# Kernel tuning notes

Hardware: AMD Instinct MI355X
Metric: run time of the kernel (lower is better)

## Reference

```python
import jax, jax.numpy as jnp
import numpy as np

NF = 10      # num RBF / Chebyshev features
GAMMA = 1.0
EMB = 10
H = 64
NHEADS = 2


def _rbf(d):
    centers = jnp.arange(1, NF + 1, dtype=d.dtype)
    return jnp.exp(-GAMMA * (centers - d[..., None]) ** 2)


def _cheb(a):
    feats = [jnp.ones_like(a), a]
    for _ in range(2, NF):
        feats.append(2 * a * feats[-1] - feats[-2])
    return jnp.stack(feats, -1)


def _gru_layer(xs, wih, whh, bih, bhh):
    # xs: [L, B, D] -> [L, B, H]; PyTorch gate order r, z, n
    B = xs.shape[1]
    def step(h, xt):
        gi = xt @ wih.T + bih
        gh = h @ whh.T + bhh
        ir, iz, inn = jnp.split(gi, 3, -1)
        hr, hz, hn = jnp.split(gh, 3, -1)
        r = jax.nn.sigmoid(ir + hr)
        z = jax.nn.sigmoid(iz + hz)
        n = jnp.tanh(inn + r * hn)
        hnew = (1 - z) * n + z * h
        return hnew, hnew
    h0 = jnp.zeros((B, H), xs.dtype)
    _, ys = jax.lax.scan(step, h0, xs)
    return ys


def _mha(x, in_w, in_b, out_w, out_b):
    B, L, E = x.shape
    hd = E // NHEADS
    qkv = x @ in_w.T + in_b
    q, k, v = jnp.split(qkv, 3, -1)
    sp = lambda t: t.reshape(B, L, NHEADS, hd).transpose(0, 2, 1, 3)
    q, k, v = sp(q), sp(k), sp(v)
    scale = 1.0 / float(np.sqrt(hd))
    att = jax.nn.softmax(jnp.einsum('bhqd,bhkd->bhqk', q, k) * scale, -1)
    o = jnp.einsum('bhqk,bhkd->bhqd', att, v).transpose(0, 2, 1, 3).reshape(B, L, E)
    return o @ out_w.T + out_b


def _ln(x, s, b):
    m = x.mean(-1, keepdims=True)
    v = ((x - m) ** 2).mean(-1, keepdims=True)
    return (x - m) / jnp.sqrt(v + 1e-5) * s + b


def setup_inputs() -> dict:
    key = jax.random.key(0)
    ks = jax.random.split(key, 48)
    N, L = 384, 256
    # bond rows: [atom_idx1, atom_idx2, bond_dist]; angle rows: [d1, d2, angle]
    idx1 = jax.random.randint(ks[0], (N, L), 1, 119).astype(jnp.float32)
    idx2 = jax.random.randint(ks[1], (N, L), 1, 119).astype(jnp.float32)
    dist = jax.random.uniform(ks[2], (N, L), minval=0.5, maxval=5.0)
    d1 = jax.random.uniform(ks[3], (N, L), minval=0.5, maxval=5.0)
    d2 = jax.random.uniform(ks[4], (N, L), minval=0.5, maxval=5.0)
    ang = jax.random.uniform(ks[5], (N, L), minval=-1.0, maxval=1.0)
    bond_x = jnp.stack([idx1, idx2, dist], 1)
    angle_x = jnp.stack([d1, d2, ang], 1)
    is_angle = (jnp.arange(N) % 3 == 2)
    x = jnp.where(is_angle[:, None, None], angle_x, bond_x)

    def nrm(k, shp, s=0.1):
        return jax.random.normal(k, shp) * s

    D_IN = 2 * EMB + NF  # 30
    inp = {
        'x': x,
        'emb': nrm(ks[6], (119, EMB), 1.0),
        'wih0': nrm(ks[7], (3 * H, D_IN)),
        'whh0': nrm(ks[8], (3 * H, H)),
        'bih0': nrm(ks[9], (3 * H,)),
        'bhh0': nrm(ks[10], (3 * H,)),
        'wih12': nrm(ks[11], (2, 3 * H, H)),
        'whh12': nrm(ks[12], (2, 3 * H, H)),
        'bih12': nrm(ks[13], (2, 3 * H)),
        'bhh12': nrm(ks[14], (2, 3 * H)),
        'in_w1': nrm(ks[15], (3 * H, H)),
        'in_b1': nrm(ks[16], (3 * H,)),
        'out_w1': nrm(ks[17], (H, H)),
        'out_b1': nrm(ks[18], (H,)),
        'in_w2': nrm(ks[19], (3 * H, H)),
        'in_b2': nrm(ks[20], (3 * H,)),
        'out_w2': nrm(ks[21], (H, H)),
        'out_b2': nrm(ks[22], (H,)),
        'ff_w1': nrm(ks[23], (1024, H)),
        'ff_b1': nrm(ks[24], (1024,)),
        'ff_w2': nrm(ks[25], (H, 1024)),
        'ff_b2': nrm(ks[26], (H,)),
        'ln1_s': jnp.ones((H,)), 'ln1_b': jnp.zeros((H,)),
        'ln2_s': jnp.ones((H,)), 'ln2_b': jnp.zeros((H,)),
        'ln3_s': jnp.ones((H,)), 'ln3_b': jnp.zeros((H,)),
        'ln4_s': jnp.ones((H,)), 'ln4_b': jnp.zeros((H,)),
        'fw1': nrm(ks[27], (256, H)), 'fb1': nrm(ks[28], (256,)),
        'fw2': nrm(ks[29], (64, 256)), 'fb2': nrm(ks[30], (64,)),
        'fw3': nrm(ks[31], (32, 64)), 'fb3': nrm(ks[32], (32,)),
        'fw4': nrm(ks[33], (1, 32)), 'fb4': nrm(ks[34], (1,)),
    }
    return inp


def reference(x, emb, wih0, whh0, bih0, bhh0, wih12, whh12, bih12, bhh12,
              in_w1, in_b1, out_w1, out_b1, in_w2, in_b2, out_w2, out_b2,
              ff_w1, ff_b1, ff_w2, ff_b2,
              ln1_s, ln1_b, ln2_s, ln2_b, ln3_s, ln3_b, ln4_s, ln4_b,
              fw1, fb1, fw2, fb2, fw3, fb3, fw4, fb4):
    # Vectorized featurization (replaces the per-triplet Python loop):
    # rows with i%3 in {0,1} are bond rows, i%3==2 are angle rows.
    i1 = jnp.clip(x[:, 0].astype(jnp.int32), 0, 118)
    i2 = jnp.clip(x[:, 1].astype(jnp.int32), 0, 118)
    bond_feat = jnp.concatenate([emb[i1], emb[i2], _rbf(x[:, 2])], -1)
    angle_feat = jnp.concatenate([_rbf(x[:, 0]), _rbf(x[:, 1]), _cheb(x[:, 2])], -1)
    is_angle = (jnp.arange(x.shape[0]) % 3 == 2)
    feat = jnp.where(is_angle[:, None, None], angle_feat, bond_feat)  # [N, L, 30]

    hs = feat.transpose(1, 0, 2)  # [L, N, 30]
    hs = _gru_layer(hs, wih0, whh0, bih0, bhh0)
    for l in range(2):
        hs = _gru_layer(hs, wih12[l], whh12[l], bih12[l], bhh12[l])
    g = hs.transpose(1, 0, 2)  # [N, L, H]

    def ffn(t):
        return jax.nn.relu(jax.nn.relu(t @ ff_w1.T + ff_b1) @ ff_w2.T + ff_b2)

    a = _mha(g, in_w1, in_b1, out_w1, out_b1)
    h = _ln(g + a, ln1_s, ln1_b)
    h = _ln(h + ffn(h), ln2_s, ln2_b)
    a = _mha(h, in_w2, in_b2, out_w2, out_b2)
    h = _ln(a + a, ln3_s, ln3_b)  # faithful to original: attn_out + attn_out
    h = _ln(h + ffn(h), ln4_s, ln4_b)
    o = h[:, -1, :]
    o = jax.nn.silu(o @ fw1.T + fb1)
    o = jax.nn.silu(o @ fw2.T + fb2)
    o = jax.nn.silu(o @ fw3.T + fb3)
    o = o @ fw4.T + fb4
    return o.squeeze(-1)
```

## Files before the change

### kernel.cpp

```cpp
#include <hip/hip_runtime.h>

static constexpr int NB   = 384;
static constexpr int SEQL = 256;
static constexpr int NROWS = NB * SEQL;

typedef short bf16x8 __attribute__((ext_vector_type(8)));
typedef float f32x4  __attribute__((ext_vector_type(4)));

union B8u {
    bf16x8 v;
    ushort us[8];
    uint4  q;
};

union F4u { float4 v; float f[4]; };

__device__ inline ushort f2bf(float f) {
    uint u = __float_as_uint(f);
    uint r = u + 0x7FFFu + ((u >> 16) & 1u);
    return (ushort)(r >> 16);
}

__device__ inline void split8(float4 a, float4 b, B8u& hi, B8u& lo) {
    float f[8] = {a.x, a.y, a.z, a.w, b.x, b.y, b.z, b.w};
    #pragma unroll
    for (int i = 0; i < 8; ++i) {
        ushort h = f2bf(f[i]);
        hi.us[i] = h;
        float fh = __uint_as_float(((uint)h) << 16);
        lo.us[i] = f2bf(f[i] - fh);
    }
}

__device__ inline float fast_rcp(float x) {
    float r = __builtin_amdgcn_rcpf(x);
    return r * (2.f - x * r);
}
__device__ inline float fast_sig(float x) {
    float e = __expf(fminf(-x, 80.f));
    return fast_rcp(1.f + e);
}
__device__ inline float fast_tanh(float a) {
    float e = __expf(fminf(2.f * fabsf(a), 80.f));
    float t = 1.f - 2.f * fast_rcp(1.f + e);
    return (a >= 0.f) ? t : -t;
}

__device__ inline void split1(const float* s, ushort* h, ushort* l, int i) {
    float f = s[i];
    ushort hh = f2bf(f);
    h[i] = hh;
    l[i] = f2bf(f - __uint_as_float(((uint)hh) << 16));
}

__global__ __launch_bounds__(256) void split_all(
    const float* s0, const float* s1, const float* s2, const float* s3,
    const float* s4, const float* s5, const float* s6, const float* s7,
    const float* s8,
    ushort* h0, ushort* h1, ushort* h2, ushort* h3, ushort* h4,
    ushort* h5, ushort* h6, ushort* h7, ushort* h8,
    ushort* l0, ushort* l1, ushort* l2, ushort* l3, ushort* l4,
    ushort* l5, ushort* l6, ushort* l7, ushort* l8)
{
    const int b = blockIdx.x;
    const float* s; ushort* h; ushort* l; int base;
    if      (b < 256) { s = s0; h = h0; l = l0; base = 0; }
    else if (b < 512) { s = s1; h = h1; l = l1; base = 256; }
    else if (b < 608) { s = s2; h = h2; l = l2; base = 512; }
    else if (b < 656) { s = s3; h = h3; l = l3; base = 608; }
    else if (b < 704) { s = s4; h = h4; l = l4; base = 656; }
    else if (b < 720) { s = s5; h = h5; l = l5; base = 704; }
    else if (b < 736) { s = s6; h = h6; l = l6; base = 720; }
    else if (b < 784) { s = s7; h = h7; l = l7; base = 736; }
    else              { s = s8; h = h8; l = l8; base = 784; }
    split1(s, h, l, (b - base) * 256 + threadIdx.x);
}

__global__ __launch_bounds__(192) void featproj_kernel(
    const float* __restrict__ x, const float* __restrict__ emb,
    const float* __restrict__ wih0, const float* __restrict__ bih0,
    float* __restrict__ X)
{
    __shared__ float F[32][33];
    const int tid = threadIdx.x;
    const int m0  = blockIdx.x * 32;

    if (tid < 96) {
        const int r   = tid & 31;
        const int grp = tid >> 5;
        const int m   = m0 + r;
        const int b   = m % NB;
        const int l   = m / NB;
        const float* xb = x + (size_t)b * (3 * SEQL);
        const float x0 = xb[l], x1 = xb[SEQL + l], x2 = xb[2 * SEQL + l];
        const bool is_angle = (b % 3) == 2;
        float o[10];
        if (is_angle) {
            if (grp < 2) {
                const float a = (grp == 0) ? x0 : x1;
                #pragma unroll
                for (int c = 0; c < 10; ++c) { float d = (float)(c + 1) - a; o[c] = __expf(-d * d); }
            } else {
                float t0 = 1.f, t1 = x2;
                o[0] = 1.f; o[1] = x2;
                #pragma unroll
                for (int c = 2; c < 10; ++c) { float t = 2.f * x2 * t1 - t0; o[c] = t; t0 = t1; t1 = t; }
            }
        } else {
            if (grp < 2) {
                const float xv = (grp == 0) ? x0 : x1;
                int idx = (int)xv; idx = idx < 0 ? 0 : (idx > 118 ? 118 : idx);
                #pragma unroll
                for (int c = 0; c < 10; ++c) o[c] = emb[idx * 10 + c];
            } else {
                #pragma unroll
                for (int c = 0; c < 10; ++c) { float d = (float)(c + 1) - x2; o[c] = __expf(-d * d); }
            }
        }
        #pragma unroll
        for (int c = 0; c < 10; ++c) F[r][grp * 10 + c] = o[c];
    }
    __syncthreads();

    float w[30];
    #pragma unroll
    for (int k = 0; k < 30; ++k) w[k] = wih0[tid * 30 + k];
    const float bj = bih0[tid];
    for (int r = 0; r < 32; ++r) {
        float acc = bj;
        #pragma unroll
        for (int k = 0; k < 30; ++k) acc += F[r][k] * w[k];
        X[(size_t)(m0 + r) * 192 + tid] = acc;
    }
}

__global__ __launch_bounds__(256, 1) void gru_mfma(
    const float* __restrict__ X, const ushort* __restrict__ WhhHi,
    const ushort* __restrict__ WhhLo, const float* __restrict__ bhh,
    float* __restrict__ Y, int out_batch_major)
{
    constexpr int PAD = 88;
    __shared__ __align__(16) ushort Hh[2][16][PAD];
    __shared__ __align__(16) ushort Hl[2][16][PAD];

    const int tid  = threadIdx.x;
    const int wt   = tid >> 6;
    const int lane = tid & 63;
    const int c    = lane & 15;
    const int g    = lane >> 4;
    const int b0   = blockIdx.x * 16;

    B8u awh[3][2], awl[3][2];
    #pragma unroll
    for (int gam = 0; gam < 3; ++gam)
        #pragma unroll
        for (int ks = 0; ks < 2; ++ks) {
            size_t off = (size_t)(64 * gam + 16 * wt + c) * 64 + 32 * ks + 8 * g;
            awh[gam][ks].q = *(const uint4*)(WhhHi + off);
            awl[gam][ks].q = *(const uint4*)(WhhLo + off);
        }
    float bg[3][4];
    #pragma unroll
    for (int gam = 0; gam < 3; ++gam)
        #pragma unroll
        for (int r = 0; r < 4; ++r)
            bg[gam][r] = bhh[64 * gam + 16 * wt + 4 * g + r];

    {
        ushort* zh = &Hh[0][0][0];
        ushort* zl = &Hl[0][0][0];
        for (int i = tid; i < 2 * 16 * PAD; i += 256) { zh[i] = 0; zl[i] = 0; }
    }
    float hold[4] = {0.f, 0.f, 0.f, 0.f};

    F4u gi[3];
    {
        const float* xp = X + ((size_t)(b0 + c)) * 192;
        #pragma unroll
        for (int gam = 0; gam < 3; ++gam)
            gi[gam].v = *(const float4*)(xp + 64 * gam + 16 * wt + 4 * g);
    }
    __syncthreads();

    for (int t = 0; t < SEQL; ++t) {
        const int p = t & 1;

        B8u bh[2], bl[2];
        #pragma unroll
        for (int ks = 0; ks < 2; ++ks) {
            const int sl = (4 * ks + g) ^ (c & 7);
            bh[ks].q = *(const uint4*)&Hh[p][c][sl * 8];
            bl[ks].q = *(const uint4*)&Hl[p][c][sl * 8];
        }

        f32x4 a0[3], a1[3];
        #pragma unroll
        for (int gam = 0; gam < 3; ++gam) {
            a0[gam] = (f32x4){bg[gam][0], bg[gam][1], bg[gam][2], bg[gam][3]};
            a1[gam] = (f32x4){0.f, 0.f, 0.f, 0.f};
        }
        #pragma unroll
        for (int gam = 0; gam < 3; ++gam) {
            a0[gam] = __builtin_amdgcn_mfma_f32_16x16x32_bf16(awh[gam][0].v, bh[0].v, a0[gam], 0, 0, 0);
            a1[gam] = __builtin_amdgcn_mfma_f32_16x16x32_bf16(awh[gam][1].v, bh[1].v, a1[gam], 0, 0, 0);
            a0[gam] = __builtin_amdgcn_mfma_f32_16x16x32_bf16(awl[gam][0].v, bh[0].v, a0[gam], 0, 0, 0);
            a1[gam] = __builtin_amdgcn_mfma_f32_16x16x32_bf16(awl[gam][1].v, bh[1].v, a1[gam], 0, 0, 0);
            a0[gam] = __builtin_amdgcn_mfma_f32_16x16x32_bf16(awh[gam][0].v, bl[0].v, a0[gam], 0, 0, 0);
            a1[gam] = __builtin_amdgcn_mfma_f32_16x16x32_bf16(awh[gam][1].v, bl[1].v, a1[gam], 0, 0, 0);
        }

        F4u ngi[3];
        {
            const int tn = (t + 1 < SEQL) ? t + 1 : t;
            const float* xp = X + ((size_t)tn * NB + b0 + c) * 192;
            #pragma unroll
            for (int gam = 0; gam < 3; ++gam)
                ngi[gam].v = *(const float4*)(xp + 64 * gam + 16 * wt + 4 * g);
        }

        float hn4[4];
        #pragma unroll
        for (int r = 0; r < 4; ++r) {
            const float gr = a0[0][r] + a1[0][r];
            const float gz = a0[1][r] + a1[1][r];
            const float gn = a0[2][r] + a1[2][r];
            const float rr = fast_sig(gi[0].f[r] + gr);
            const float zz = fast_sig(gi[1].f[r] + gz);
            const float nn = fast_tanh(gi[2].f[r] + rr * gn);
            hn4[r] = (1.f - zz) * nn + zz * hold[r];
            hold[r] = hn4[r];
        }

        {
            const size_t row = out_batch_major ? ((size_t)(b0 + c) * SEQL + t)
                                               : ((size_t)t * NB + b0 + c);
            *(float4*)&Y[row * 64 + 16 * wt + 4 * g] =
                make_float4(hn4[0], hn4[1], hn4[2], hn4[3]);
        }

        {
            ushort hh[4], hl[4];
            #pragma unroll
            for (int r = 0; r < 4; ++r) {
                ushort h = f2bf(hn4[r]);
                hh[r] = h;
                hl[r] = f2bf(hn4[r] - __uint_as_float(((uint)h) << 16));
            }
            const int sl = (2 * wt + (g >> 1)) ^ (c & 7);
            const int ad = sl * 8 + (g & 1) * 4;
            *(uint2*)&Hh[p ^ 1][c][ad] = make_uint2((uint)hh[0] | ((uint)hh[1] << 16),
                                                    (uint)hh[2] | ((uint)hh[3] << 16));
            *(uint2*)&Hl[p ^ 1][c][ad] = make_uint2((uint)hl[0] | ((uint)hl[1] << 16),
                                                    (uint)hl[2] | ((uint)hl[3] << 16));
        }
        #pragma unroll
        for (int gam = 0; gam < 3; ++gam) gi[gam].v = ngi[gam].v;

        asm volatile("s_waitcnt lgkmcnt(0)" ::: "memory");
        __builtin_amdgcn_sched_barrier(0);
        __builtin_amdgcn_s_barrier();
        __builtin_amdgcn_sched_barrier(0);
    }
}

template<int NCOLS>
__global__ __launch_bounds__(256, 2) void gemm_mfma(
    const float* __restrict__ A, const ushort* __restrict__ Whi,
    const ushort* __restrict__ Wlo, const float* __restrict__ bias,
    float* __restrict__ C)
{
    const int tid = threadIdx.x;
    const int w   = tid >> 6;
    const int lane = tid & 63;
    const int c = lane & 15;
    const int g = lane >> 4;
    const int m0 = blockIdx.x * 128 + 32 * w;

    B8u ah[2][2], al[2][2];
    #pragma unroll
    for (int rm = 0; rm < 2; ++rm) {
        const float* ap = A + (size_t)(m0 + 16 * rm + c) * 64;
        #pragma unroll
        for (int ks = 0; ks < 2; ++ks) {
            float4 v0 = *(const float4*)(ap + 32 * ks + 8 * g);
            float4 v1 = *(const float4*)(ap + 32 * ks + 8 * g + 4);
            split8(v0, v1, ah[rm][ks], al[rm][ks]);
        }
    }

    f32x4 acc[NCOLS / 16][2];
    #pragma unroll
    for (int nt = 0; nt < NCOLS / 16; ++nt) {
        float bv = bias[16 * nt + c];
        #pragma unroll
        for (int rm = 0; rm < 2; ++rm)
            acc[nt][rm] = (f32x4){bv, bv, bv, bv};
    }

    #pragma unroll
    for (int nt = 0; nt < NCOLS / 16; ++nt) {
        B8u wh[2], wl[2];
        #pragma unroll
        for (int ks = 0; ks < 2; ++ks) {
            size_t off = (size_t)(16 * nt + c) * 64 + 32 * ks + 8 * g;
            wh[ks].q = *(const uint4*)(Whi + off);
            wl[ks].q = *(const uint4*)(Wlo + off);
        }
        #pragma unroll
        for (int rm = 0; rm < 2; ++rm)
            #pragma unroll
            for (int ks = 0; ks < 2; ++ks) {
                acc[nt][rm] = __builtin_amdgcn_mfma_f32_16x16x32_bf16(ah[rm][ks].v, wh[ks].v, acc[nt][rm], 0, 0, 0);
                acc[nt][rm] = __builtin_amdgcn_mfma_f32_16x16x32_bf16(al[rm][ks].v, wh[ks].v, acc[nt][rm], 0, 0, 0);
                acc[nt][rm] = __builtin_amdgcn_mfma_f32_16x16x32_bf16(ah[rm][ks].v, wl[ks].v, acc[nt][rm], 0, 0, 0);
            }
    }

    #pragma unroll
    for (int nt = 0; nt < NCOLS / 16; ++nt)
        #pragma unroll
        for (int rm = 0; rm < 2; ++rm)
            #pragma unroll
            for (int reg = 0; reg < 4; ++reg) {
                int row = m0 + 16 * rm + 4 * g + reg;
                C[(size_t)row * NCOLS + 16 * nt + c] = acc[nt][rm][reg];
            }
}

__global__ __launch_bounds__(256, 2) void gemm_ln_mfma(
    const float* __restrict__ A, const ushort* __restrict__ Whi,
    const ushort* __restrict__ Wlo, const float* __restrict__ bias,
    const float* __restrict__ resid,
    const float* __restrict__ lns, const float* __restrict__ lnb,
    float* __restrict__ O)
{
    const int tid = threadIdx.x;
    const int w   = tid >> 6;
    const int lane = tid & 63;
    const int c = lane & 15;
    const int g = lane >> 4;
    const int m0 = blockIdx.x * 128 + 32 * w;

    B8u ah[2][2], al[2][2];
    #pragma unroll
    for (int rm = 0; rm < 2; ++rm) {
        const float* ap = A + (size_t)(m0 + 16 * rm + c) * 64;
        #pragma unroll
        for (int ks = 0; ks < 2; ++ks) {
            float4 v0 = *(const float4*)(ap + 32 * ks + 8 * g);
            float4 v1 = *(const float4*)(ap + 32 * ks + 8 * g + 4);
            split8(v0, v1, ah[rm][ks], al[rm][ks]);
        }
    }

    f32x4 acc[4][2];
    #pragma unroll
    for (int nt = 0; nt < 4; ++nt) {
        float bv = bias[16 * nt + c];
        #pragma unroll
        for (int rm = 0; rm < 2; ++rm)
            acc[nt][rm] = (f32x4){bv, bv, bv, bv};
    }

    #pragma unroll
    for (int nt = 0; nt < 4; ++nt) {
        B8u wh[2], wl[2];
        #pragma unroll
        for (int ks = 0; ks < 2; ++ks) {
            size_t off = (size_t)(16 * nt + c) * 64 + 32 * ks + 8 * g;
            wh[ks].q = *(const uint4*)(Whi + off);
            wl[ks].q = *(const uint4*)(Wlo + off);
        }
        #pragma unroll
        for (int rm = 0; rm < 2; ++rm)
            #pragma unroll
            for (int ks = 0; ks < 2; ++ks) {
                acc[nt][rm] = __builtin_amdgcn_mfma_f32_16x16x32_bf16(ah[rm][ks].v, wh[ks].v, acc[nt][rm], 0, 0, 0);
                acc[nt][rm] = __builtin_amdgcn_mfma_f32_16x16x32_bf16(al[rm][ks].v, wh[ks].v, acc[nt][rm], 0, 0, 0);
                acc[nt][rm] = __builtin_amdgcn_mfma_f32_16x16x32_bf16(ah[rm][ks].v, wl[ks].v, acc[nt][rm], 0, 0, 0);
            }
    }

    float vv[4][2][4];
    #pragma unroll
    for (int nt = 0; nt < 4; ++nt)
        #pragma unroll
        for (int rm = 0; rm < 2; ++rm)
            #pragma unroll
            for (int reg = 0; reg < 4; ++reg) {
                const int row = m0 + 16 * rm + 4 * g + reg;
                const float a = acc[nt][rm][reg];
                const float r_ = resid ? resid[(size_t)row * 64 + 16 * nt + c] : a;
                vv[nt][rm][reg] = a + r_;
            }

    float sv[4], bv[4];
    #pragma unroll
    for (int nt = 0; nt < 4; ++nt) { sv[nt] = lns[16 * nt + c]; bv[nt] = lnb[16 * nt + c]; }

    #pragma unroll
    for (int rm = 0; rm < 2; ++rm)
        #pragma unroll
        for (int reg = 0; reg < 4; ++reg) {
            float sum = vv[0][rm][reg] + vv[1][rm][reg] + vv[2][rm][reg] + vv[3][rm][reg];
            float sq  = vv[0][rm][reg]*vv[0][rm][reg] + vv[1][rm][reg]*vv[1][rm][reg]
                      + vv[2][rm][reg]*vv[2][rm][reg] + vv[3][rm][reg]*vv[3][rm][reg];
            #pragma unroll
            for (int off = 1; off < 16; off <<= 1) {
                sum += __shfl_xor(sum, off);
                sq  += __shfl_xor(sq,  off);
            }
            const float mean = sum * (1.f / 64.f);
            const float var  = sq * (1.f / 64.f) - mean * mean;
            const float inv  = rsqrtf(var + 1e-5f);
            const int row = m0 + 16 * rm + 4 * g + reg;
            #pragma unroll
            for (int nt = 0; nt < 4; ++nt)
                O[(size_t)row * 64 + 16 * nt + c] =
                    (vv[nt][rm][reg] - mean) * inv * sv[nt] + bv[nt];
        }
}

__global__ __launch_bounds__(256, 2) void ffn_ln_mfma(
    const float* __restrict__ Xin,
    const ushort* __restrict__ W1hi, const ushort* __restrict__ W1lo,
    const ushort* __restrict__ W2hi, const ushort* __restrict__ W2lo,
    const float* __restrict__ b1, const float* __restrict__ b2,
    const float* __restrict__ lns, const float* __restrict__ lnb,
    float* __restrict__ Out)
{
    __shared__ __align__(16) ushort sW1h[64 * 72], sW1l[64 * 72];
    __shared__ __align__(16) ushort sW2h[64 * 72], sW2l[64 * 72];
    __shared__ __align__(16) ushort sHh[128 * 72], sHl[128 * 72];
    __shared__ float sb1[64];

    const int tid = threadIdx.x;
    const int w   = tid >> 6;
    const int lane = tid & 63;
    const int c = lane & 15;
    const int g = lane >> 4;
    const int r0 = blockIdx.x * 128;

    B8u xh[2][2], xl[2][2];
    #pragma unroll
    for (int rm = 0; rm < 2; ++rm) {
        const float* ap = Xin + (size_t)(r0 + 32 * w + 16 * rm + c) * 64;
        #pragma unroll
        for (int ks = 0; ks < 2; ++ks) {
            float4 v0 = *(const float4*)(ap + 32 * ks + 8 * g);
            float4 v1 = *(const float4*)(ap + 32 * ks + 8 * g + 4);
            split8(v0, v1, xh[rm][ks], xl[rm][ks]);
        }
    }

    f32x4 acc2[4][2];
    #pragma unroll
    for (int jt = 0; jt < 4; ++jt) {
        float bv = b2[16 * jt + c];
        #pragma unroll
        for (int mt = 0; mt < 2; ++mt)
            acc2[jt][mt] = (f32x4){bv, bv, bv, bv};
    }

    for (int nc = 0; nc < 16; ++nc) {
        __syncthreads();
        {
            const int n = tid >> 2, s = tid & 3;
            size_t s1 = (size_t)(nc * 64 + n) * 64 + s * 16;
            size_t s2 = (size_t)n * 1024 + nc * 64 + s * 16;
            int d = n * 72 + s * 16;
            *(uint4*)&sW1h[d]     = *(const uint4*)(W1hi + s1);
            *(uint4*)&sW1h[d + 8] = *(const uint4*)(W1hi + s1 + 8);
            *(uint4*)&sW1l[d]     = *(const uint4*)(W1lo + s1);
            *(uint4*)&sW1l[d + 8] = *(const uint4*)(W1lo + s1 + 8);
            *(uint4*)&sW2h[d]     = *(const uint4*)(W2hi + s2);
            *(uint4*)&sW2h[d + 8] = *(const uint4*)(W2hi + s2 + 8);
            *(uint4*)&sW2l[d]     = *(const uint4*)(W2lo + s2);
            *(uint4*)&sW2l[d + 8] = *(const uint4*)(W2lo + s2 + 8);
            if (tid < 64) sb1[tid] = b1[nc * 64 + tid];
        }
        __syncthreads();

        f32x4 acc1[4][2];
        #pragma unroll
        for (int jm = 0; jm < 4; ++jm) {
            float b0 = sb1[16 * jm + 4 * g + 0];
            float b1v = sb1[16 * jm + 4 * g + 1];
            float b2v = sb1[16 * jm + 4 * g + 2];
            float b3v = sb1[16 * jm + 4 * g + 3];
            #pragma unroll
            for (int rm = 0; rm < 2; ++rm)
                acc1[jm][rm] = (f32x4){b0, b1v, b2v, b3v};
        }
        #pragma unroll
        for (int jm = 0; jm < 4; ++jm) {
            B8u w1h[2], w1l[2];
            #pragma unroll
            for (int ks = 0; ks < 2; ++ks) {
                int off = (16 * jm + c) * 72 + 32 * ks + 8 * g;
                w1h[ks].q = *(const uint4*)&sW1h[off];
                w1l[ks].q = *(const uint4*)&sW1l[off];
            }
            #pragma unroll
            for (int rm = 0; rm < 2; ++rm)
                #pragma unroll
                for (int ks = 0; ks < 2; ++ks) {
                    acc1[jm][rm] = __builtin_amdgcn_mfma_f32_16x16x32_bf16(w1h[ks].v, xh[rm][ks].v, acc1[jm][rm], 0, 0, 0);
                    acc1[jm][rm] = __builtin_amdgcn_mfma_f32_16x16x32_bf16(w1l[ks].v, xh[rm][ks].v, acc1[jm][rm], 0, 0, 0);
                    acc1[jm][rm] = __builtin_amdgcn_mfma_f32_16x16x32_bf16(w1h[ks].v, xl[rm][ks].v, acc1[jm][rm], 0, 0, 0);
                }
        }
        #pragma unroll
        for (int jm = 0; jm < 4; ++jm)
            #pragma unroll
            for (int rm = 0; rm < 2; ++rm) {
                ushort hh[4], hl[4];
                #pragma unroll
                for (int reg = 0; reg < 4; ++reg) {
                    float hv = fmaxf(acc1[jm][rm][reg], 0.f);
                    ushort h = f2bf(hv);
                    hh[reg] = h;
                    float fh = __uint_as_float(((uint)h) << 16);
                    hl[reg] = f2bf(hv - fh);
                }
                int el = (32 * w + 16 * rm + c) * 72 + 16 * jm + 4 * g;
                *(uint2*)&sHh[el] = make_uint2((uint)hh[0] | ((uint)hh[1] << 16),
                                               (uint)hh[2] | ((uint)hh[3] << 16));
                *(uint2*)&sHl[el] = make_uint2((uint)hl[0] | ((uint)hl[1] << 16),
                                               (uint)hl[2] | ((uint)hl[3] << 16));
            }
        asm volatile("s_waitcnt lgkmcnt(0)" ::: "memory");
        __builtin_amdgcn_sched_barrier(0);

        #pragma unroll
        for (int ks = 0; ks < 2; ++ks) {
            B8u ahh[2], ahl[2], bwh[4], bwl[4];
            #pragma unroll
            for (int mt = 0; mt < 2; ++mt) {
                int el = (32 * w + 16 * mt + c) * 72 + 32 * ks + 8 * g;
                ahh[mt].q = *(const uint4*)&sHh[el];
                ahl[mt].q = *(const uint4*)&sHl[el];
            }
            #pragma unroll
            for (int jt = 0; jt < 4; ++jt) {
                int el = (16 * jt + c) * 72 + 32 * ks + 8 * g;
                bwh[jt].q = *(const uint4*)&sW2h[el];
                bwl[jt].q = *(const uint4*)&sW2l[el];
            }
            #pragma unroll
            for (int jt = 0; jt < 4; ++jt)
                #pragma unroll
                for (int mt = 0; mt < 2; ++mt) {
                    acc2[jt][mt] = __builtin_amdgcn_mfma_f32_16x16x32_bf16(ahh[mt].v, bwh[jt].v, acc2[jt][mt], 0, 0, 0);
                    acc2[jt][mt] = __builtin_amdgcn_mfma_f32_16x16x32_bf16(ahl[mt].v, bwh[jt].v, acc2[jt][mt], 0, 0, 0);
                    acc2[jt][mt] = __builtin_amdgcn_mfma_f32_16x16x32_bf16(ahh[mt].v, bwl[jt].v, acc2[jt][mt], 0, 0, 0);
                }
        }
    }

    float vv[4][2][4];
    #pragma unroll
    for (int jt = 0; jt < 4; ++jt)
        #pragma unroll
        for (int mt = 0; mt < 2; ++mt)
            #pragma unroll
            for (int reg = 0; reg < 4; ++reg) {
                const int row = r0 + 32 * w + 16 * mt + 4 * g + reg;
                vv[jt][mt][reg] = fmaxf(acc2[jt][mt][reg], 0.f) +
                                  Xin[(size_t)row * 64 + 16 * jt + c];
            }

    float sv[4], bv[4];
    #pragma unroll
    for (int jt = 0; jt < 4; ++jt) { sv[jt] = lns[16 * jt + c]; bv[jt] = lnb[16 * jt + c]; }

    #pragma unroll
    for (int mt = 0; mt < 2; ++mt)
        #pragma unroll
        for (int reg = 0; reg < 4; ++reg) {
            float sum = vv[0][mt][reg] + vv[1][mt][reg] + vv[2][mt][reg] + vv[3][mt][reg];
            float sq  = vv[0][mt][reg]*vv[0][mt][reg] + vv[1][mt][reg]*vv[1][mt][reg]
                      + vv[2][mt][reg]*vv[2][mt][reg] + vv[3][mt][reg]*vv[3][mt][reg];
            #pragma unroll
            for (int off = 1; off < 16; off <<= 1) {
                sum += __shfl_xor(sum, off);
                sq  += __shfl_xor(sq,  off);
            }
            const float mean = sum * (1.f / 64.f);
            const float var  = sq * (1.f / 64.f) - mean * mean;
            const float inv  = rsqrtf(var + 1e-5f);
            const int row = r0 + 32 * w + 16 * mt + 4 * g + reg;
            #pragma unroll
            for (int jt = 0; jt < 4; ++jt)
                Out[(size_t)row * 64 + 16 * jt + c] =
                    (vv[jt][mt][reg] - mean) * inv * sv[jt] + bv[jt];
        }
}

__global__ __launch_bounds__(256, 2) void attn_mfma(
    const float* __restrict__ QKV, float* __restrict__ Out)
{
    __shared__ __align__(16) ushort Ph[4][4096];
    __shared__ __align__(16) ushort Pl[4][4096];

    const int h = blockIdx.x;
    const int b = blockIdx.y;
    const int tid = threadIdx.x;
    const int w = tid >> 6;
    const int lane = tid & 63;
    const int c = lane & 15;
    const int g = lane >> 4;
    const float scale = 0.17677669529663687f;

    const float* base = QKV + (size_t)b * SEQL * 192;
    ushort* phw = Ph[w];
    ushort* plw = Pl[w];

    B8u qh[4], ql[4];
    #pragma unroll
    for (int qt = 0; qt < 4; ++qt) {
        const float* p = base + (size_t)(64 * w + 16 * qt + c) * 192 + h * 32 + 8 * g;
        float4 v0 = *(const float4*)p;
        float4 v1 = *(const float4*)(p + 4);
        v0.x *= scale; v0.y *= scale; v0.z *= scale; v0.w *= scale;
        v1.x *= scale; v1.y *= scale; v1.z *= scale; v1.w *= scale;
        split8(v0, v1, qh[qt], ql[qt]);
    }

    f32x4 o[2][4];
    #pragma unroll
    for (int dt = 0; dt < 2; ++dt)
        #pragma unroll
        for (int qt = 0; qt < 4; ++qt)
            o[dt][qt] = (f32x4){0.f, 0.f, 0.f, 0.f};
    float mrun[4] = {-1e30f, -1e30f, -1e30f, -1e30f};
    float lrun[4] = {0.f, 0.f, 0.f, 0.f};

    for (int kc = 0; kc < 4; ++kc) {
        B8u kh[4], kl[4];
        #pragma unroll
        for (int kt = 0; kt < 4; ++kt) {
            const float* p = base + (size_t)(kc * 64 + 16 * kt + c) * 192 + 64 + h * 32 + 8 * g;
            split8(*(const float4*)p, *(const float4*)(p + 4), kh[kt], kl[kt]);
        }
        f32x4 st[4][4];
        #pragma unroll
        for (int kt = 0; kt < 4; ++kt)
            #pragma unroll
            for (int qt = 0; qt < 4; ++qt)
                st[kt][qt] = (f32x4){0.f, 0.f, 0.f, 0.f};
        #pragma unroll
        for (int kt = 0; kt < 4; ++kt)
            #pragma unroll
            for (int qt = 0; qt < 4; ++qt) {
                st[kt][qt] = __builtin_amdgcn_mfma_f32_16x16x32_bf16(kh[kt].v, qh[qt].v, st[kt][qt], 0, 0, 0);
                st[kt][qt] = __builtin_amdgcn_mfma_f32_16x16x32_bf16(kl[kt].v, qh[qt].v, st[kt][qt], 0, 0, 0);
                st[kt][qt] = __builtin_amdgcn_mfma_f32_16x16x32_bf16(kh[kt].v, ql[qt].v, st[kt][qt], 0, 0, 0);
            }

        asm volatile("s_waitcnt lgkmcnt(0)" ::: "memory");
        #pragma unroll
        for (int qt = 0; qt < 4; ++qt) {
            float cmax = st[0][qt][0];
            #pragma unroll
            for (int kt = 0; kt < 4; ++kt)
                #pragma unroll
                for (int r = 0; r < 4; ++r) cmax = fmaxf(cmax, st[kt][qt][r]);
            cmax = fmaxf(cmax, __shfl_xor(cmax, 16));
            cmax = fmaxf(cmax, __shfl_xor(cmax, 32));
            const float mnew = fmaxf(mrun[qt], cmax);
            const float corr = __expf(mrun[qt] - mnew);
            mrun[qt] = mnew;
            const int ql_ = 16 * qt + c;
            float csum = 0.f;
            #pragma unroll
            for (int kt = 0; kt < 4; ++kt) {
                ushort hh[4], hl[4];
                #pragma unroll
                for (int r = 0; r < 4; ++r) {
                    float pv = __expf(st[kt][qt][r] - mnew);
                    csum += pv;
                    ushort ph_ = f2bf(pv);
                    hh[r] = ph_;
                    hl[r] = f2bf(pv - __uint_as_float(((uint)ph_) << 16));
                }
                const int ow = (2 * kt + (g >> 1)) ^ (ql_ & 7);
                const int addr = ql_ * 64 + ow * 8 + (g & 1) * 4;
                *(uint2*)&phw[addr] = make_uint2((uint)hh[0] | ((uint)hh[1] << 16),
                                                 (uint)hh[2] | ((uint)hh[3] << 16));
                *(uint2*)&plw[addr] = make_uint2((uint)hl[0] | ((uint)hl[1] << 16),
                                                 (uint)hl[2] | ((uint)hl[3] << 16));
            }
            csum += __shfl_xor(csum, 16);
            csum += __shfl_xor(csum, 32);
            lrun[qt] = lrun[qt] * corr + csum;
            #pragma unroll
            for (int dt = 0; dt < 2; ++dt)
                #pragma unroll
                for (int r = 0; r < 4; ++r) o[dt][qt][r] *= corr;
        }

        B8u vh[2][2], vl[2][2];
        #pragma unroll
        for (int ks = 0; ks < 2; ++ks)
            #pragma unroll
            for (int dt = 0; dt < 2; ++dt) {
                const float* vp = base + (size_t)(kc * 64 + ks * 32 + 8 * g) * 192 + 128 + h * 32 + 16 * dt + c;
                float f0 = vp[0], f1 = vp[192], f2 = vp[384], f3 = vp[576];
                float f4 = vp[768], f5 = vp[960], f6 = vp[1152], f7 = vp[1344];
                split8(make_float4(f0, f1, f2, f3), make_float4(f4, f5, f6, f7),
                       vh[ks][dt], vl[ks][dt]);
            }

        asm volatile("s_waitcnt lgkmcnt(0)" ::: "memory");
        __builtin_amdgcn_sched_barrier(0);

        #pragma unroll
        for (int ks = 0; ks < 2; ++ks)
            #pragma unroll
            for (int qt = 0; qt < 4; ++qt) {
                const int ql_ = 16 * qt + c;
                const int orr = (ks * 4 + g) ^ (ql_ & 7);
                const int addr = ql_ * 64 + orr * 8;
                B8u pbh, pbl;
                pbh.q = *(const uint4*)&phw[addr];
                pbl.q = *(const uint4*)&plw[addr];
                #pragma unroll
                for (int dt = 0; dt < 2; ++dt) {
                    o[dt][qt] = __builtin_amdgcn_mfma_f32_16x16x32_bf16(vh[ks][dt].v, pbh.v, o[dt][qt], 0, 0, 0);
                    o[dt][qt] = __builtin_amdgcn_mfma_f32_16x16x32_bf16(vl[ks][dt].v, pbh.v, o[dt][qt], 0, 0, 0);
                    o[dt][qt] = __builtin_amdgcn_mfma_f32_16x16x32_bf16(vh[ks][dt].v, pbl.v, o[dt][qt], 0, 0, 0);
                }
            }
    }

    #pragma unroll
    for (int qt = 0; qt < 4; ++qt) {
        const float inv = 1.f / lrun[qt];
        const size_t row = (size_t)b * SEQL + 64 * w + 16 * qt + c;
        #pragma unroll
        for (int dt = 0; dt < 2; ++dt)
            #pragma unroll
            for (int r = 0; r < 4; ++r)
                Out[row * 64 + h * 32 + 16 * dt + 4 * g + r] = o[dt][qt][r] * inv;
    }
}

__global__ __launch_bounds__(256) void head_kernel(
    const float* __restrict__ Hf,
    const float* __restrict__ fw1, const float* __restrict__ fb1,
    const float* __restrict__ fw2, const float* __restrict__ fb2,
    const float* __restrict__ fw3, const float* __restrict__ fb3,
    const float* __restrict__ fw4, const float* __restrict__ fb4,
    float* __restrict__ out)
{
    const int b = blockIdx.x;
    const int tid = threadIdx.x;
    __shared__ float t0[64], t1[256], t2[64], t3[32];
    if (tid < 64) t0[tid] = Hf[((size_t)b * SEQL + (SEQL - 1)) * 64 + tid];
    __syncthreads();
    {
        float acc = fb1[tid];
        #pragma unroll 4
        for (int k = 0; k < 64; ++k) acc += t0[k] * fw1[tid * 64 + k];
        t1[tid] = acc / (1.f + __expf(-acc));
    }
    __syncthreads();
    if (tid < 64) {
        float acc = fb2[tid];
        #pragma unroll 4
        for (int k = 0; k < 256; ++k) acc += t1[k] * fw2[tid * 256 + k];
        t2[tid] = acc / (1.f + __expf(-acc));
    }
    __syncthreads();
    if (tid < 32) {
        float acc = fb3[tid];
        #pragma unroll 4
        for (int k = 0; k < 64; ++k) acc += t2[k] * fw3[tid * 64 + k];
        t3[tid] = acc / (1.f + __expf(-acc));
    }
    __syncthreads();
    if (tid == 0) {
        float acc = fb4[0];
        #pragma unroll
        for (int k = 0; k < 32; ++k) acc += t3[k] * fw4[k];
        out[b] = acc;
    }
}

extern "C" void kernel_launch(void* const* d_in, const int* in_sizes, int n_in,
                              void* d_out, int out_size, void* d_ws, size_t ws_size,
                              hipStream_t stream) {
    const float* x     = (const float*)d_in[0];
    const float* emb   = (const float*)d_in[1];
    const float* wih0  = (const float*)d_in[2];
    const float* whh0  = (const float*)d_in[3];
    const float* bih0  = (const float*)d_in[4];
    const float* bhh0  = (const float*)d_in[5];
    const float* wih12 = (const float*)d_in[6];
    const float* whh12 = (const float*)d_in[7];
    const float* bih12 = (const float*)d_in[8];
    const float* bhh12 = (const float*)d_in[9];
    const float* in_w1 = (const float*)d_in[10];
    const float* in_b1 = (const float*)d_in[11];
    const float* out_w1= (const float*)d_in[12];
    const float* out_b1= (const float*)d_in[13];
    const float* in_w2 = (const float*)d_in[14];
    const float* in_b2 = (const float*)d_in[15];
    const float* out_w2= (const float*)d_in[16];
    const float* out_b2= (const float*)d_in[17];
    const float* ff_w1 = (const float*)d_in[18];
    const float* ff_b1 = (const float*)d_in[19];
    const float* ff_w2 = (const float*)d_in[20];
    const float* ff_b2 = (const float*)d_in[21];
    const float* ln1_s = (const float*)d_in[22];
    const float* ln1_b = (const float*)d_in[23];
    const float* ln2_s = (const float*)d_in[24];
    const float* ln2_b = (const float*)d_in[25];
    const float* ln3_s = (const float*)d_in[26];
    const float* ln3_b = (const float*)d_in[27];
    const float* ln4_s = (const float*)d_in[28];
    const float* ln4_b = (const float*)d_in[29];
    const float* fw1   = (const float*)d_in[30];
    const float* fb1   = (const float*)d_in[31];
    const float* fw2   = (const float*)d_in[32];
    const float* fb2   = (const float*)d_in[33];
    const float* fw3   = (const float*)d_in[34];
    const float* fb3   = (const float*)d_in[35];
    const float* fw4   = (const float*)d_in[36];
    const float* fb4   = (const float*)d_in[37];

    float* ws = (float*)d_ws;
    float* X  = ws;
    float* S0 = X  + (size_t)NROWS * 192;
    float* S1 = S0 + (size_t)NROWS * 64;
    float* S2 = S1 + (size_t)NROWS * 64;

    ushort* bf = (ushort*)(S2 + (size_t)NROWS * 64);
    ushort* ffw1hi = bf;
    ushort* ffw1lo = ffw1hi + 65536;
    ushort* ffw2hi = ffw1lo + 65536;
    ushort* ffw2lo = ffw2hi + 65536;
    ushort* wghi   = ffw2lo + 65536;
    ushort* wglo   = wghi + 24576;
    ushort* q1hi   = wglo + 24576;
    ushort* q1lo   = q1hi + 12288;
    ushort* q2hi   = q1lo + 12288;
    ushort* q2lo   = q2hi + 12288;
    ushort* o1hi   = q2lo + 12288;
    ushort* o1lo   = o1hi + 4096;
    ushort* o2hi   = o1lo + 4096;
    ushort* o2lo   = o2hi + 4096;
    ushort* w0hi   = o2lo + 4096;
    ushort* w0lo   = w0hi + 12288;
    ushort* w12hi  = w0lo + 12288;
    ushort* w12lo  = w12hi + 24576;

    split_all<<<880, 256, 0, stream>>>(
        ff_w1, ff_w2, wih12, in_w1, in_w2, out_w1, out_w2, whh0, whh12,
        ffw1hi, ffw2hi, wghi, q1hi, q2hi, o1hi, o2hi, w0hi, w12hi,
        ffw1lo, ffw2lo, wglo, q1lo, q2lo, o1lo, o2lo, w0lo, w12lo);

    featproj_kernel<<<NROWS / 32, 192, 0, stream>>>(x, emb, wih0, bih0, X);
    gru_mfma<<<NB / 16, 256, 0, stream>>>(X, w0hi, w0lo, bhh0, S0, 0);
    gemm_mfma<192><<<NROWS / 128, 256, 0, stream>>>(S0, wghi, wglo, bih12, X);
    gru_mfma<<<NB / 16, 256, 0, stream>>>(X, w12hi, w12lo, bhh12, S1, 0);
    gemm_mfma<192><<<NROWS / 128, 256, 0, stream>>>(S1, wghi + 12288, wglo + 12288, bih12 + 192, X);
    gru_mfma<<<NB / 16, 256, 0, stream>>>(X, w12hi + 12288, w12lo + 12288, bhh12 + 192, S0, 1);

    gemm_mfma<192><<<NROWS / 128, 256, 0, stream>>>(S0, q1hi, q1lo, in_b1, X);
    attn_mfma<<<dim3(2, NB), 256, 0, stream>>>(X, S1);
    gemm_ln_mfma<<<NROWS / 128, 256, 0, stream>>>(S1, o1hi, o1lo, out_b1,
                                                  S0, ln1_s, ln1_b, S2);
    ffn_ln_mfma<<<NROWS / 128, 256, 0, stream>>>(S2, ffw1hi, ffw1lo, ffw2hi, ffw2lo,
                                                 ff_b1, ff_b2, ln2_s, ln2_b, S0);

    gemm_mfma<192><<<NROWS / 128, 256, 0, stream>>>(S0, q2hi, q2lo, in_b2, X);
    attn_mfma<<<dim3(2, NB), 256, 0, stream>>>(X, S1);
    gemm_ln_mfma<<<NROWS / 128, 256, 0, stream>>>(S1, o2hi, o2lo, out_b2,
                                                  nullptr, ln3_s, ln3_b, S2);
    ffn_ln_mfma<<<NROWS / 128, 256, 0, stream>>>(S2, ffw1hi, ffw1lo, ffw2hi, ffw2lo,
                                                 ff_b1, ff_b2, ln4_s, ln4_b, S1);

    head_kernel<<<NB, 256, 0, stream>>>(S1, fw1, fb1, fw2, fb2, fw3, fb3, fw4, fb4,
                                        (float*)d_out);
    (void)in_sizes; (void)n_in; (void)out_size; (void)ws_size;
}
```

Baseline: 1.055 ms.

## Fuse next GRU layer input projection into the recurrent GRU kernel

The GRU kernel now also computes the next layer's input-gate projection (W_ih·h + b_ih) with MFMA. At step t it reuses the h_{t-1} bf16 hi/lo fragments already loaded from LDS, and handles the last timestep after the loop. This removes the two standalone gemm launches between GRU layers and skips writing and re-reading the intermediate hidden-state sequence. In exchange, every serial timestep issues extra MFMAs and 192-wide stores inside the latency-bound recurrence, which may lengthen the critical path. The intermediate buffer reuses the contiguous S0..S2 workspace with a 192-wide stride.

New measurement: 1.383 ms. 31.0% more time.

```diff
diff --git a/kernel.cpp b/kernel.cpp
--- a/kernel.cpp
+++ b/kernel.cpp
@@ -137,7 +137,9 @@
 __global__ __launch_bounds__(256, 1) void gru_mfma(
     const float* __restrict__ X, const ushort* __restrict__ WhhHi,
     const ushort* __restrict__ WhhLo, const float* __restrict__ bhh,
-    float* __restrict__ Y, int out_batch_major)
+    float* __restrict__ Y, int out_batch_major,
+    const ushort* __restrict__ WIhi, const ushort* __restrict__ WIlo,
+    const float* __restrict__ bih_next, float* __restrict__ Xout, int do_proj)
 {
     constexpr int PAD = 88;
     __shared__ __align__(16) ushort Hh[2][16][PAD];
@@ -165,6 +167,24 @@
         #pragma unroll
         for (int r = 0; r < 4; ++r)
             bg[gam][r] = bhh[64 * gam + 16 * wt + 4 * g + r];
+
+    B8u pwh[3][2], pwl[3][2];
+    float bg2[3][4];
+    if (do_proj) {
+        #pragma unroll
+        for (int gam = 0; gam < 3; ++gam)
+            #pragma unroll
+            for (int ks = 0; ks < 2; ++ks) {
+                size_t off = (size_t)(64 * gam + 16 * wt + c) * 64 + 32 * ks + 8 * g;
+                pwh[gam][ks].q = *(const uint4*)(WIhi + off);
+                pwl[gam][ks].q = *(const uint4*)(WIlo + off);
+            }
+        #pragma unroll
+        for (int gam = 0; gam < 3; ++gam)
+            #pragma unroll
+            for (int r = 0; r < 4; ++r)
+                bg2[gam][r] = bih_next[64 * gam + 16 * wt + 4 * g + r];
+    }
 
     {
         ushort* zh = &Hh[0][0][0];
@@ -207,6 +227,27 @@
             a1[gam] = __builtin_amdgcn_mfma_f32_16x16x32_bf16(awl[gam][1].v, bh[1].v, a1[gam], 0, 0, 0);
             a0[gam] = __builtin_amdgcn_mfma_f32_16x16x32_bf16(awh[gam][0].v, bl[0].v, a0[gam], 0, 0, 0);
             a1[gam] = __builtin_amdgcn_mfma_f32_16x16x32_bf16(awh[gam][1].v, bl[1].v, a1[gam], 0, 0, 0);
+        }
+
+        if (do_proj && t > 0) {
+            f32x4 pa[3];
+            #pragma unroll
+            for (int gam = 0; gam < 3; ++gam)
+                pa[gam] = (f32x4){bg2[gam][0], bg2[gam][1], bg2[gam][2], bg2[gam][3]};
+            #pragma unroll
+            for (int gam = 0; gam < 3; ++gam) {
+                pa[gam] = __builtin_amdgcn_mfma_f32_16x16x32_bf16(pwh[gam][0].v, bh[0].v, pa[gam], 0, 0, 0);
+                pa[gam] = __builtin_amdgcn_mfma_f32_16x16x32_bf16(pwh[gam][1].v, bh[1].v, pa[gam], 0, 0, 0);
+                pa[gam] = __builtin_amdgcn_mfma_f32_16x16x32_bf16(pwl[gam][0].v, bh[0].v, pa[gam], 0, 0, 0);
+                pa[gam] = __builtin_amdgcn_mfma_f32_16x16x32_bf16(pwl[gam][1].v, bh[1].v, pa[gam], 0, 0, 0);
+                pa[gam] = __builtin_amdgcn_mfma_f32_16x16x32_bf16(pwh[gam][0].v, bl[0].v, pa[gam], 0, 0, 0);
+                pa[gam] = __builtin_amdgcn_mfma_f32_16x16x32_bf16(pwh[gam][1].v, bl[1].v, pa[gam], 0, 0, 0);
+            }
+            const size_t prow = (size_t)(t - 1) * NB + b0 + c;
+            #pragma unroll
+            for (int gam = 0; gam < 3; ++gam)
+                *(float4*)&Xout[prow * 192 + 64 * gam + 16 * wt + 4 * g] =
+                    make_float4(pa[gam][0], pa[gam][1], pa[gam][2], pa[gam][3]);
         }
 
         F4u ngi[3];
@@ -231,7 +272,7 @@
             hold[r] = hn4[r];
         }
 
-        {
+        if (Y) {
             const size_t row = out_batch_major ? ((size_t)(b0 + c) * SEQL + t)
                                                : ((size_t)t * NB + b0 + c);
             *(float4*)&Y[row * 64 + 16 * wt + 4 * g] =
@@ -260,6 +301,35 @@
         __builtin_amdgcn_sched_barrier(0);
         __builtin_amdgcn_s_barrier();
         __builtin_amdgcn_sched_barrier(0);
+    }
+
+    if (do_proj) {
+        const int p = SEQL & 1;
+        B8u bh[2], bl[2];
+        #pragma unroll
+        for (int ks = 0; ks < 2; ++ks) {
+            const int sl = (4 * ks + g) ^ (c & 7);
+            bh[ks].q = *(const uint4*)&Hh[p][c][sl * 8];
+            bl[ks].q = *(const uint4*)&Hl[p][c][sl * 8];
+        }
+        f32x4 pa[3];
+        #pragma unroll
+        for (int gam = 0; gam < 3; ++gam)
+            pa[gam] = (f32x4){bg2[gam][0], bg2[gam][1], bg2[gam][2], bg2[gam][3]};
+        #pragma unroll
+        for (int gam = 0; gam < 3; ++gam) {
+            pa[gam] = __builtin_amdgcn_mfma_f32_16x16x32_bf16(pwh[gam][0].v, bh[0].v, pa[gam], 0, 0, 0);
+            pa[gam] = __builtin_amdgcn_mfma_f32_16x16x32_bf16(pwh[gam][1].v, bh[1].v, pa[gam], 0, 0, 0);
+            pa[gam] = __builtin_amdgcn_mfma_f32_16x16x32_bf16(pwl[gam][0].v, bh[0].v, pa[gam], 0, 0, 0);
+            pa[gam] = __builtin_amdgcn_mfma_f32_16x16x32_bf16(pwl[gam][1].v, bh[1].v, pa[gam], 0, 0, 0);
+            pa[gam] = __builtin_amdgcn_mfma_f32_16x16x32_bf16(pwh[gam][0].v, bl[0].v, pa[gam], 0, 0, 0);
+            pa[gam] = __builtin_amdgcn_mfma_f32_16x16x32_bf16(pwh[gam][1].v, bl[1].v, pa[gam], 0, 0, 0);
+        }
+        const size_t prow = (size_t)(SEQL - 1) * NB + b0 + c;
+        #pragma unroll
+        for (int gam = 0; gam < 3; ++gam)
+            *(float4*)&Xout[prow * 192 + 64 * gam + 16 * wt + 4 * g] =
+                make_float4(pa[gam][0], pa[gam][1], pa[gam][2], pa[gam][3]);
     }
 }
 
@@ -835,6 +905,7 @@
     float* S0 = X  + (size_t)NROWS * 192;
     float* S1 = S0 + (size_t)NROWS * 64;
     float* S2 = S1 + (size_t)NROWS * 64;
+    float* Xmid = S0;
 
     ushort* bf = (ushort*)(S2 + (size_t)NROWS * 64);
     ushort* ffw1hi = bf;
@@ -862,11 +933,16 @@
         ffw1lo, ffw2lo, wglo, q1lo, q2lo, o1lo, o2lo, w0lo, w12lo);
 
     featproj_kernel<<<NROWS / 32, 192, 0, stream>>>(x, emb, wih0, bih0, X);
-    gru_mfma<<<NB / 16, 256, 0, stream>>>(X, w0hi, w0lo, bhh0, S0, 0);
-    gemm_mfma<192><<<NROWS / 128, 256, 0, stream>>>(S0, wghi, wglo, bih12, X);
-    gru_mfma<<<NB / 16, 256, 0, stream>>>(X, w12hi, w12lo, bhh12, S1, 0);
-    gemm_mfma<192><<<NROWS / 128, 256, 0, stream>>>(S1, wghi + 12288, wglo + 12288, bih12 + 192, X);
-    gru_mfma<<<NB / 16, 256, 0, stream>>>(X, w12hi + 12288, w12lo + 12288, bhh12 + 192, S0, 1);
+    gru_mfma<<<NB / 16, 256, 0, stream>>>(X, w0hi, w0lo, bhh0,
+                                          nullptr, 0,
+                                          wghi, wglo, bih12, Xmid, 1);
+    gru_mfma<<<NB / 16, 256, 0, stream>>>(Xmid, w12hi, w12lo, bhh12,
+                                          nullptr, 0,
+                                          wghi + 12288, wglo + 12288,
+                                          bih12 + 192, X, 1);
+    gru_mfma<<<NB / 16, 256, 0, stream>>>(X, w12hi + 12288, w12lo + 12288,
+                                          bhh12 + 192, S0, 1,
+                                          nullptr, nullptr, nullptr, nullptr, 0);
 
     gemm_mfma<192><<<NROWS / 128, 256, 0, stream>>>(S0, q1hi, q1lo, in_b1, X);
     attn_mfma<<<dim3(2, NB), 256, 0, stream>>>(X, S1);
```
